# Kernel optimization log

Hardware: AMD Instinct MI355X
Metric: run time of the kernel (lower is better)

Reference implementation:

```python
import jax, jax.numpy as jnp
import numpy as np

N, D, E = 50000, 128, 800000


def setup_inputs() -> dict:
    key = jax.random.key(0)
    ks = jax.random.split(key, 12)
    x0 = jax.random.normal(ks[0], (N, D), dtype=jnp.float32)
    x1 = jax.random.normal(ks[1], (N, D), dtype=jnp.float32)
    edge_index = jax.random.randint(ks[2], (2, E), 0, N, dtype=jnp.int64)
    s = 0.05
    W1 = jax.random.normal(ks[3], (D, D), dtype=jnp.float32) * s
    b1 = jax.random.normal(ks[4], (D,), dtype=jnp.float32) * s
    W2 = jax.random.normal(ks[5], (D, D), dtype=jnp.float32) * s
    b2 = jax.random.normal(ks[6], (D,), dtype=jnp.float32) * s
    a1_w = jax.random.normal(ks[7], (D,), dtype=jnp.float32) * s
    a1_b = jax.random.normal(ks[8], (), dtype=jnp.float32) * s
    a2_w = jax.random.normal(ks[9], (D,), dtype=jnp.float32) * s
    a2_b = jax.random.normal(ks[10], (), dtype=jnp.float32) * s
    return {"x0": x0, "x1": x1, "edge_index": edge_index,
            "W1": W1, "b1": b1, "W2": W2, "b2": b2,
            "a1_w": a1_w, "a1_b": a1_b, "a2_w": a2_w, "a2_b": a2_b}


def reference(x0, x1, edge_index, W1, b1, W2, b2, a1_w, a1_b, a2_w, a2_b):
    # LeakyReLU(0.2) applied to both projections
    lrelu = lambda v: jnp.where(v >= 0, v, 0.2 * v)
    x0_i = lrelu(x0 @ W1.T + b1)          # [N, D]
    x0_j = lrelu(x0 @ W2.T + b2)          # [N, D]
    a1 = x0_i @ a1_w + a1_b               # [N]
    a2 = x0_j @ a2_w + a2_b               # [N]
    src, dst = edge_index[0], edge_index[1]
    # sigmoid(a_1 + a_2.T) evaluated only at the sparse edge indices
    att = jax.nn.sigmoid(a1[src] + a2[dst])            # [E]
    msg = att[:, None] * x0_j[dst]                     # [E, D]
    out = jax.ops.segment_sum(msg, src, num_segments=x0.shape[0])  # sparse.mm
    return out + x0
```

## Files before the change

### kernel.cpp

```cpp
#include <hip/hip_runtime.h>
#include <hip/hip_bf16.h>

typedef unsigned int u32;
typedef unsigned short u16;

#define DIM 128
#define CHUNK 2048

typedef __bf16 bfrag __attribute__((ext_vector_type(8)));
typedef float  facc  __attribute__((ext_vector_type(4)));

__device__ __forceinline__ float2 bfpair(u32 u) {
    union { u32 i; float f; } lo, hi;
    lo.i = (u & 0xFFFFu) << 16;
    hi.i = u & 0xFFFF0000u;
    return make_float2(lo.f, hi.f);
}
__device__ __forceinline__ float bf1(u16 h) {
    union { u32 i; float f; } a; a.i = ((u32)h) << 16; return a.f;
}
__device__ __forceinline__ u16 f2bf(float f) {
    __hip_bfloat16 h = __float2bfloat16(f);
    return *reinterpret_cast<u16*>(&h);
}
__device__ __forceinline__ u32 packbf(float x, float y) {
    return (u32)f2bf(x) | ((u32)f2bf(y) << 16);
}

template<bool BF16>
__device__ __forceinline__ float ldf(const void* p, int i) {
    if constexpr (BF16) return bf1(((const u16*)p)[i]);
    else                return ((const float*)p)[i];
}

template<bool BF16>
__device__ __forceinline__ bfrag ldfrag(const void* base, int row, int elt) {
    if constexpr (BF16) {
        const uint4* p = (const uint4*)((const u16*)base + (size_t)row * DIM + elt);
        return __builtin_bit_cast(bfrag, *p);
    } else {
        const float4* p = (const float4*)((const float*)base + (size_t)row * DIM + elt);
        float4 f0 = p[0], f1 = p[1];
        uint4 u = make_uint4(packbf(f0.x, f0.y), packbf(f0.z, f0.w),
                             packbf(f1.x, f1.y), packbf(f1.z, f1.w));
        return __builtin_bit_cast(bfrag, u);
    }
}

__global__ __launch_bounds__(64) void sniff_kernel(const u32* __restrict__ x0w,
                                                   const int* __restrict__ eiw,
                                                   int* __restrict__ flags) {
    int l = threadIdx.x;
    u32 w = x0w[l];
    u32 ef = (w >> 7) & 0xFF;
    bool inr = (ef >= 99 && ef <= 141);
    unsigned long long m1 = __ballot(inr);
    bool zodd = (eiw[2 * l + 1] == 0);
    unsigned long long m2 = __ballot(zodd);
    if (l == 0) {
        flags[0] = (__popcll(m1) >= 48) ? 1 : 0;
        flags[1] = (__popcll(m2) >= 32) ? 1 : 0;
    }
}

template<bool BF16>
__device__ __forceinline__ void proj_body(
    int grp, int chunk, int l,
    const void* __restrict__ x0v,
    const void* __restrict__ W1v, const void* __restrict__ b1v,
    const void* __restrict__ W2v, const void* __restrict__ b2v,
    const void* __restrict__ a1wv, const void* __restrict__ a1bv,
    const void* __restrict__ a2wv, const void* __restrict__ a2bv,
    u16* __restrict__ xj, float* __restrict__ a1, float* __restrict__ a2,
    int n)
{
    const void* Wv  = grp ? W2v  : W1v;
    const void* bv  = grp ? b2v  : b1v;
    const void* awv = grp ? a2wv : a1wv;
    const void* abv = grp ? a2bv : a1bv;
    float* aout     = grp ? a2   : a1;

    const int r0 = chunk * 32;
    const int lr = l & 15;
    const int q  = l >> 4;

    bfrag a[2][4];
    #pragma unroll
    for (int rt = 0; rt < 2; ++rt) {
        int row = min(r0 + rt * 16 + lr, n - 1);
        #pragma unroll
        for (int k = 0; k < 4; ++k)
            a[rt][k] = ldfrag<BF16>(x0v, row, k * 32 + q * 8);
    }

    facc acc[2][8];
    #pragma unroll
    for (int rt = 0; rt < 2; ++rt)
        #pragma unroll
        for (int ct = 0; ct < 8; ++ct)
            acc[rt][ct] = (facc){0.f, 0.f, 0.f, 0.f};

    #pragma unroll
    for (int ct = 0; ct < 8; ++ct) {
        bfrag bb[4];
        #pragma unroll
        for (int k = 0; k < 4; ++k)
            bb[k] = ldfrag<BF16>(Wv, ct * 16 + lr, k * 32 + q * 8);
        #pragma unroll
        for (int rt = 0; rt < 2; ++rt)
            #pragma unroll
            for (int k = 0; k < 4; ++k)
                acc[rt][ct] = __builtin_amdgcn_mfma_f32_16x16x32_bf16(
                    a[rt][k], bb[k], acc[rt][ct], 0, 0, 0);
    }

    float s[2][4] = {{0.f,0.f,0.f,0.f},{0.f,0.f,0.f,0.f}};
    #pragma unroll
    for (int ct = 0; ct < 8; ++ct) {
        float bc  = ldf<BF16>(bv,  ct * 16 + lr);
        float awc = ldf<BF16>(awv, ct * 16 + lr);
        #pragma unroll
        for (int rt = 0; rt < 2; ++rt)
            #pragma unroll
            for (int reg = 0; reg < 4; ++reg) {
                float v = acc[rt][ct][reg] + bc;
                v = v >= 0.f ? v : 0.2f * v;
                int row = r0 + rt * 16 + q * 4 + reg;
                if (grp && row < n)
                    xj[(size_t)row * DIM + ct * 16 + lr] = f2bf(v);
                s[rt][reg] = fmaf(v, awc, s[rt][reg]);
            }
    }
    #pragma unroll
    for (int off = 1; off < 16; off <<= 1)
        #pragma unroll
        for (int rt = 0; rt < 2; ++rt)
            #pragma unroll
            for (int reg = 0; reg < 4; ++reg)
                s[rt][reg] += __shfl_xor(s[rt][reg], off);
    if (lr == 0) {
        float ab = ldf<BF16>(abv, 0);
        #pragma unroll
        for (int rt = 0; rt < 2; ++rt)
            #pragma unroll
            for (int reg = 0; reg < 4; ++reg) {
                int row = r0 + rt * 16 + q * 4 + reg;
                if (row < n) aout[row] = s[rt][reg] + ab;
            }
    }
}

__global__ __launch_bounds__(64) void proj64_kernel(
    const void* __restrict__ x0v,
    const void* __restrict__ W1v, const void* __restrict__ b1v,
    const void* __restrict__ W2v, const void* __restrict__ b2v,
    const void* __restrict__ a1wv, const void* __restrict__ a1bv,
    const void* __restrict__ a2wv, const void* __restrict__ a2bv,
    u16* __restrict__ xj, float* __restrict__ a1, float* __restrict__ a2,
    const int* __restrict__ flags, int n, int nchunk)
{
    const int b = blockIdx.x;
    const int grp = (b >= nchunk) ? 1 : 0;
    const int chunk = b - grp * nchunk;
    const int l = threadIdx.x;
    if (flags[0] != 0)
        proj_body<true >(grp, chunk, l, x0v, W1v, b1v, W2v, b2v, a1wv, a1bv,
                         a2wv, a2bv, xj, a1, a2, n);
    else
        proj_body<false>(grp, chunk, l, x0v, W1v, b1v, W2v, b2v, a1wv, a1bv,
                         a2wv, a2bv, xj, a1, a2, n);
}

__global__ __launch_bounds__(256) void countH_kernel(
    const int* __restrict__ ei, u32* __restrict__ keys0,
    int* __restrict__ cnt, const int* __restrict__ flags, int ne, int nblk)
{
    __shared__ int h[256];
    const int b = blockIdx.x, t = threadIdx.x;
    h[t] = 0;
    __syncthreads();
    const bool i64 = flags[1] != 0;
    const int base = b * CHUNK;
    #pragma unroll
    for (int r = 0; r < CHUNK / 256; ++r) {
        int i = base + r * 256 + t;
        if (i < ne) {
            int src = i64 ? ei[2 * i] : ei[i];
            int dst = i64 ? ei[2 * (ne + i)] : ei[ne + i];
            u32 key = ((u32)src << 16) | (u32)dst;
            keys0[i] = key;
            atomicAdd(&h[key >> 24], 1);
        }
    }
    __syncthreads();
    cnt[t * nblk + b] = h[t];
}

__global__ __launch_bounds__(256) void scan1_kernel(
    const int* __restrict__ cnt, int* __restrict__ off,
    int* __restrict__ tot, int nblk)
{
    __shared__ int v[512];
    const int d = blockIdx.x, t = threadIdx.x;
    int c0 = (t < nblk) ? cnt[d * nblk + t] : 0;
    int c1 = (t + 256 < nblk) ? cnt[d * nblk + t + 256] : 0;
    v[t] = c0; v[t + 256] = c1;
    __syncthreads();
    for (int s = 1; s < 512; s <<= 1) {
        int a0 = v[t],      b0 = (t >= s) ? v[t - s] : 0;
        int a1 = v[t + 256], b1 = (t + 256 >= s) ? v[t + 256 - s] : 0;
        __syncthreads();
        v[t] = a0 + b0; v[t + 256] = a1 + b1;
        __syncthreads();
    }
    if (t < nblk)       off[d * nblk + t]       = v[t] - c0;
    if (t + 256 < nblk) off[d * nblk + t + 256] = v[t + 256] - c1;
    if (t == 0) tot[d] = v[511];
}

__global__ __launch_bounds__(256) void scan2_kernel(
    const int* __restrict__ tot, int* __restrict__ basev)
{
    __shared__ int v[256];
    const int t = threadIdx.x;
    int c = tot[t];
    v[t] = c;
    __syncthreads();
    for (int s = 1; s < 256; s <<= 1) {
        int a = v[t], b = (t >= s) ? v[t - s] : 0;
        __syncthreads();
        v[t] = a + b;
        __syncthreads();
    }
    basev[t] = v[t] - c;
}

__global__ __launch_bounds__(256) void reorderH_kernel(
    const u32* __restrict__ kin, u32* __restrict__ kout,
    const int* __restrict__ off, const int* __restrict__ basev,
    int ne, int nblk)
{
    __shared__ int boff[256];
    __shared__ int bcnt[256];
    const int b = blockIdx.x, t = threadIdx.x;
    const int base = b * CHUNK;
    boff[t] = basev[t] + off[t * nblk + b];
    bcnt[t] = 0;
    __syncthreads();
    #pragma unroll
    for (int r = 0; r < CHUNK / 256; ++r) {
        int i = base + r * 256 + t;
        if (i < ne) {
            u32 key = kin[i];
            int d = key >> 24;
            int rk = atomicAdd(&bcnt[d], 1);
            kout[boff[d] + rk] = key;
        }
    }
}

__global__ __launch_bounds__(256) void bucket_kernel(
    const u32* __restrict__ keys1, const int* __restrict__ basev,
    const int* __restrict__ tot, const float* __restrict__ a1,
    const float* __restrict__ a2, int* __restrict__ ptr,
    u32* __restrict__ sorted, int n)
{
    __shared__ int cnt[256];
    __shared__ int sc[256];
    __shared__ int cur[256];
    const int b = blockIdx.x, t = threadIdx.x;
    const int base = basev[b];
    const int size = tot[b];
    cnt[t] = 0;
    __syncthreads();
    for (int i = t; i < size; i += 256)
        atomicAdd(&cnt[(keys1[base + i] >> 16) & 0xFF], 1);
    __syncthreads();
    int c = cnt[t];
    sc[t] = c;
    __syncthreads();
    for (int s = 1; s < 256; s <<= 1) {
        int a = sc[t], add = (t >= s) ? sc[t - s] : 0;
        __syncthreads();
        sc[t] = a + add;
        __syncthreads();
    }
    int ex = sc[t] - c;
    cur[t] = ex;
    int sg = (b << 8) + t;
    if (sg <= n) ptr[sg] = base + ex;
    __syncthreads();
    for (int i = t; i < size; i += 256) {
        u32 key = keys1[base + i];
        int j   = (key >> 16) & 0xFF;
        int rk  = atomicAdd(&cur[j], 1);
        int src = (int)(key >> 16);
        int dst = (int)(key & 0xFFFFu);
        float av  = a1[src] + a2[dst];
        float att = 1.0f / (1.0f + __expf(-av));
        u32 a16 = (u32)lrintf(att * 65535.0f);
        sorted[base + rk] = (a16 << 16) | (u32)dst;
    }
}

#define ATTDEC(r) ((float)((r) >> 16) * (1.0f / 65535.0f))

__global__ __launch_bounds__(256) void gather_kernel(
    const int* __restrict__ ptr, const u32* __restrict__ sorted,
    const u32* __restrict__ xjw, const void* __restrict__ x0v,
    void* __restrict__ outv, const int* __restrict__ flags, int n)
{
    const bool bf16 = flags[0] != 0;
    int s = blockIdx.x * 4 + (threadIdx.x >> 6);
    int l = threadIdx.x & 63;
    if (s >= n) return;

    float2 acc0, acc1;
    if (bf16) acc0 = bfpair(((const u32*)x0v)[(size_t)s * 64 + l]);
    else      acc0 = ((const float2*)x0v)[(size_t)s * 64 + l];
    acc1 = make_float2(0.f, 0.f);

    int k = ptr[s], end = ptr[s + 1];

    while (k + 16 <= end) {
        u32 r[16];
        #pragma unroll
        for (int j = 0; j < 16; ++j) r[j] = sorted[k + j];
        u32 w[16];
        #pragma unroll
        for (int j = 0; j < 16; ++j) w[j] = xjw[(size_t)(r[j] & 0xFFFFu) * 64 + l];
        #pragma unroll
        for (int j = 0; j < 16; ++j) {
            float att = ATTDEC(r[j]);
            float2 xv = bfpair(w[j]);
            if (j & 1) { acc1.x = fmaf(att, xv.x, acc1.x);
                         acc1.y = fmaf(att, xv.y, acc1.y); }
            else       { acc0.x = fmaf(att, xv.x, acc0.x);
                         acc0.y = fmaf(att, xv.y, acc0.y); }
        }
        k += 16;
    }
    if (k + 8 <= end) {
        u32 r[8];
        #pragma unroll
        for (int j = 0; j < 8; ++j) r[j] = sorted[k + j];
        u32 w[8];
        #pragma unroll
        for (int j = 0; j < 8; ++j) w[j] = xjw[(size_t)(r[j] & 0xFFFFu) * 64 + l];
        #pragma unroll
        for (int j = 0; j < 8; ++j) {
            float att = ATTDEC(r[j]);
            float2 xv = bfpair(w[j]);
            if (j & 1) { acc1.x = fmaf(att, xv.x, acc1.x);
                         acc1.y = fmaf(att, xv.y, acc1.y); }
            else       { acc0.x = fmaf(att, xv.x, acc0.x);
                         acc0.y = fmaf(att, xv.y, acc0.y); }
        }
        k += 8;
    }
    if (k + 4 <= end) {
        u32 r[4];
        #pragma unroll
        for (int j = 0; j < 4; ++j) r[j] = sorted[k + j];
        u32 w[4];
        #pragma unroll
        for (int j = 0; j < 4; ++j) w[j] = xjw[(size_t)(r[j] & 0xFFFFu) * 64 + l];
        #pragma unroll
        for (int j = 0; j < 4; ++j) {
            float att = ATTDEC(r[j]);
            float2 xv = bfpair(w[j]);
            if (j & 1) { acc1.x = fmaf(att, xv.x, acc1.x);
                         acc1.y = fmaf(att, xv.y, acc1.y); }
            else       { acc0.x = fmaf(att, xv.x, acc0.x);
                         acc0.y = fmaf(att, xv.y, acc0.y); }
        }
        k += 4;
    }
    for (; k < end; ++k) {
        u32 cur = sorted[k];
        float att = ATTDEC(cur);
        float2 xv = bfpair(xjw[(size_t)(cur & 0xFFFFu) * 64 + l]);
        acc0.x = fmaf(att, xv.x, acc0.x);
        acc0.y = fmaf(att, xv.y, acc0.y);
    }
    acc0.x += acc1.x;
    acc0.y += acc1.y;

    if (bf16) ((u32*)outv)[(size_t)s * 64 + l] = packbf(acc0.x, acc0.y);
    else      ((float2*)outv)[(size_t)s * 64 + l] = acc0;
}

extern "C" void kernel_launch(void* const* d_in, const int* in_sizes, int n_in,
                              void* d_out, int out_size, void* d_ws, size_t ws_size,
                              hipStream_t stream)
{
    const void* x0  = d_in[0];
    const int*  ei  = (const int*)d_in[2];
    const void* W1  = d_in[3];
    const void* b1  = d_in[4];
    const void* W2  = d_in[5];
    const void* b2  = d_in[6];
    const void* a1w = d_in[7];
    const void* a1b = d_in[8];
    const void* a2w = d_in[9];
    const void* a2b = d_in[10];

    const int n = in_sizes[0] / DIM;
    const int e = in_sizes[2] / 2;
    const int nblk = (e + CHUNK - 1) / CHUNK;

    char* ws = (char*)d_ws;
    int* flags = (int*)ws;
    size_t off = 1024;
    u16* xj = (u16*)(ws + off);
    off += (size_t)n * DIM * sizeof(u16);   off = (off + 255) & ~(size_t)255;
    float* a1 = (float*)(ws + off);
    off += (size_t)n * sizeof(float);       off = (off + 255) & ~(size_t)255;
    float* a2 = (float*)(ws + off);
    off += (size_t)n * sizeof(float);       off = (off + 255) & ~(size_t)255;
    u32* keys0 = (u32*)(ws + off);
    off += (size_t)e * sizeof(u32);         off = (off + 255) & ~(size_t)255;
    u32* keys1 = (u32*)(ws + off);
    off += (size_t)e * sizeof(u32);         off = (off + 255) & ~(size_t)255;
    int* cntH = (int*)(ws + off);
    off += (size_t)256 * nblk * sizeof(int); off = (off + 255) & ~(size_t)255;
    int* offH = (int*)(ws + off);
    off += (size_t)256 * nblk * sizeof(int); off = (off + 255) & ~(size_t)255;
    int* totH = (int*)(ws + off);  off += 1024;
    int* baseH = (int*)(ws + off); off += 1024;
    int* ptr = (int*)(ws + off);
    off += (size_t)(n + 1) * sizeof(int);   off = (off + 255) & ~(size_t)255;
    u32* sorted = (u32*)(ws + off);

    sniff_kernel<<<1, 64, 0, stream>>>((const u32*)x0, ei, flags);

    const int nchunk = (n + 31) / 32;

    proj64_kernel<<<2 * nchunk, 64, 0, stream>>>(x0, W1, b1, W2, b2, a1w, a1b,
        a2w, a2b, xj, a1, a2, flags, n, nchunk);

    countH_kernel<<<nblk, 256, 0, stream>>>(ei, keys0, cntH, flags, e, nblk);
    scan1_kernel<<<256, 256, 0, stream>>>(cntH, offH, totH, nblk);
    scan2_kernel<<<1, 256, 0, stream>>>(totH, baseH);
    reorderH_kernel<<<nblk, 256, 0, stream>>>(keys0, keys1, offH, baseH, e, nblk);
    const int nbucket = (n >> 8) + 1;
    bucket_kernel<<<nbucket, 256, 0, stream>>>(keys1, baseH, totH, a1, a2,
                                               ptr, sorted, n);

    int gblocks = (n + 3) / 4;
    gather_kernel<<<gblocks, 256, 0, stream>>>(ptr, sorted, (const u32*)xj,
                                               x0, d_out, flags, n);
}
```

Baseline: 209.9 us.

## Pre-convert x0/W to bf16 and stage weights in LDS for projection

Adds a conversion kernel that turns fp32 x0 and W1/W2 into bf16 copies in workspace. The projection kernel now uses 256-thread blocks: each block stages the 128x128 bf16 weight matrix into padded shared memory once, and four waves reuse it, instead of every wave reloading weight fragments from global memory. The aim is to cut redundant weight loads and per-fragment fp32 to bf16 packing. The cost is an extra pass over x0 (read fp32, write bf16, then read bf16 again) and an extra launch.

```diff
diff --git a/kernel.cpp b/kernel.cpp
--- a/kernel.cpp
+++ b/kernel.cpp
@@ -5,6 +5,7 @@
 typedef unsigned short u16;
 
 #define DIM 128
+#define LWS 136
 #define CHUNK 2048
 
 typedef __bf16 bfrag __attribute__((ext_vector_type(8)));
@@ -26,25 +27,8 @@
 __device__ __forceinline__ u32 packbf(float x, float y) {
     return (u32)f2bf(x) | ((u32)f2bf(y) << 16);
 }
-
-template<bool BF16>
-__device__ __forceinline__ float ldf(const void* p, int i) {
-    if constexpr (BF16) return bf1(((const u16*)p)[i]);
-    else                return ((const float*)p)[i];
-}
-
-template<bool BF16>
-__device__ __forceinline__ bfrag ldfrag(const void* base, int row, int elt) {
-    if constexpr (BF16) {
-        const uint4* p = (const uint4*)((const u16*)base + (size_t)row * DIM + elt);
-        return __builtin_bit_cast(bfrag, *p);
-    } else {
-        const float4* p = (const float4*)((const float*)base + (size_t)row * DIM + elt);
-        float4 f0 = p[0], f1 = p[1];
-        uint4 u = make_uint4(packbf(f0.x, f0.y), packbf(f0.z, f0.w),
-                             packbf(f1.x, f1.y), packbf(f1.z, f1.w));
-        return __builtin_bit_cast(bfrag, u);
-    }
+__device__ __forceinline__ float ldfr(const void* p, int i, bool isbf) {
+    return isbf ? bf1(((const u16*)p)[i]) : ((const float*)p)[i];
 }
 
 __global__ __launch_bounds__(64) void sniff_kernel(const u32* __restrict__ x0w,
@@ -63,23 +47,63 @@
     }
 }
 
-template<bool BF16>
-__device__ __forceinline__ void proj_body(
-    int grp, int chunk, int l,
-    const void* __restrict__ x0v,
+__global__ __launch_bounds__(256) void cvt_kernel(
+    const float* __restrict__ x0, const float* __restrict__ W1,
+    const float* __restrict__ W2, u16* __restrict__ x0c, u16* __restrict__ Wc,
+    const int* __restrict__ flags, int nx)
+{
+    if (flags[0] != 0) return;
+    int i = blockIdx.x * 256 + threadIdx.x;
+    if (i >= nx + 4096) return;
+    const float* src; u16* dst; int c;
+    if (i < nx) { src = x0; dst = x0c; c = i; }
+    else {
+        int j = i - nx;
+        src = (j < 2048) ? W1 : W2;
+        dst = Wc + ((j < 2048) ? 0 : 16384);
+        c = j & 2047;
+    }
+    float4 f0 = ((const float4*)src)[c * 2];
+    float4 f1 = ((const float4*)src)[c * 2 + 1];
+    uint4 u = make_uint4(packbf(f0.x, f0.y), packbf(f0.z, f0.w),
+                         packbf(f1.x, f1.y), packbf(f1.z, f1.w));
+    ((uint4*)dst)[c] = u;
+}
+
+__global__ __launch_bounds__(256) void proj_kernel(
+    const void* __restrict__ x0v, const u16* __restrict__ x0c,
     const void* __restrict__ W1v, const void* __restrict__ b1v,
     const void* __restrict__ W2v, const void* __restrict__ b2v,
     const void* __restrict__ a1wv, const void* __restrict__ a1bv,
     const void* __restrict__ a2wv, const void* __restrict__ a2bv,
+    const u16* __restrict__ Wc,
     u16* __restrict__ xj, float* __restrict__ a1, float* __restrict__ a2,
-    int n)
-{
-    const void* Wv  = grp ? W2v  : W1v;
+    const int* __restrict__ flags, int n, int nchunk, int bpg)
+{
+    __shared__ u16 lw[128 * LWS];
+
+    const bool isbf = flags[0] != 0;
+    const int t   = threadIdx.x;
+    const int grp = blockIdx.x / bpg;
+    const int cb  = blockIdx.x % bpg;
+
+    const u16* x0s  = isbf ? (const u16*)x0v : x0c;
+    const u16* Ws   = isbf ? (const u16*)(grp ? W2v : W1v) : (Wc + grp * 16384);
     const void* bv  = grp ? b2v  : b1v;
     const void* awv = grp ? a2wv : a1wv;
     const void* abv = grp ? a2bv : a1bv;
     float* aout     = grp ? a2   : a1;
 
+    for (int j = t; j < 2048; j += 256) {
+        int r = j >> 4, c = j & 15;
+        *(uint4*)(lw + (size_t)r * LWS + c * 8) =
+            *(const uint4*)(Ws + (size_t)r * DIM + c * 8);
+    }
+    __syncthreads();
+
+    const int wid = t >> 6, l = t & 63;
+    const int chunk = cb * 4 + wid;
+    if (chunk >= nchunk) return;
     const int r0 = chunk * 32;
     const int lr = l & 15;
     const int q  = l >> 4;
@@ -89,8 +113,10 @@
     for (int rt = 0; rt < 2; ++rt) {
         int row = min(r0 + rt * 16 + lr, n - 1);
         #pragma unroll
-        for (int k = 0; k < 4; ++k)
-            a[rt][k] = ldfrag<BF16>(x0v, row, k * 32 + q * 8);
+        for (int k = 0; k < 4; ++k) {
+            const uint4* p = (const uint4*)(x0s + (size_t)row * DIM + k * 32 + q * 8);
+            a[rt][k] = __builtin_bit_cast(bfrag, *p);
+        }
     }
 
     facc acc[2][8];
@@ -103,9 +129,10 @@
     #pragma unroll
     for (int ct = 0; ct < 8; ++ct) {
         bfrag bb[4];
+        const u16* lrow = lw + (size_t)(ct * 16 + lr) * LWS;
         #pragma unroll
         for (int k = 0; k < 4; ++k)
-            bb[k] = ldfrag<BF16>(Wv, ct * 16 + lr, k * 32 + q * 8);
+            bb[k] = *(const bfrag*)(lrow + k * 32 + q * 8);
         #pragma unroll
         for (int rt = 0; rt < 2; ++rt)
             #pragma unroll
@@ -117,8 +144,8 @@
     float s[2][4] = {{0.f,0.f,0.f,0.f},{0.f,0.f,0.f,0.f}};
     #pragma unroll
     for (int ct = 0; ct < 8; ++ct) {
-        float bc  = ldf<BF16>(bv,  ct * 16 + lr);
-        float awc = ldf<BF16>(awv, ct * 16 + lr);
+        float bc  = ldfr(bv,  ct * 16 + lr, isbf);
+        float awc = ldfr(awv, ct * 16 + lr, isbf);
         #pragma unroll
         for (int rt = 0; rt < 2; ++rt)
             #pragma unroll
@@ -139,7 +166,7 @@
             for (int reg = 0; reg < 4; ++reg)
                 s[rt][reg] += __shfl_xor(s[rt][reg], off);
     if (lr == 0) {
-        float ab = ldf<BF16>(abv, 0);
+        float ab = ldfr(abv, 0, isbf);
         #pragma unroll
         for (int rt = 0; rt < 2; ++rt)
             #pragma unroll
@@ -148,27 +175,6 @@
                 if (row < n) aout[row] = s[rt][reg] + ab;
             }
     }
-}
-
-__global__ __launch_bounds__(64) void proj64_kernel(
-    const void* __restrict__ x0v,
-    const void* __restrict__ W1v, const void* __restrict__ b1v,
-    const void* __restrict__ W2v, const void* __restrict__ b2v,
-    const void* __restrict__ a1wv, const void* __restrict__ a1bv,
-    const void* __restrict__ a2wv, const void* __restrict__ a2bv,
-    u16* __restrict__ xj, float* __restrict__ a1, float* __restrict__ a2,
-    const int* __restrict__ flags, int n, int nchunk)
-{
-    const int b = blockIdx.x;
-    const int grp = (b >= nchunk) ? 1 : 0;
-    const int chunk = b - grp * nchunk;
-    const int l = threadIdx.x;
-    if (flags[0] != 0)
-        proj_body<true >(grp, chunk, l, x0v, W1v, b1v, W2v, b2v, a1wv, a1bv,
-                         a2wv, a2bv, xj, a1, a2, n);
-    else
-        proj_body<false>(grp, chunk, l, x0v, W1v, b1v, W2v, b2v, a1wv, a1bv,
-                         a2wv, a2bv, xj, a1, a2, n);
 }
 
 __global__ __launch_bounds__(256) void countH_kernel(
@@ -414,6 +420,10 @@
     size_t off = 1024;
     u16* xj = (u16*)(ws + off);
     off += (size_t)n * DIM * sizeof(u16);   off = (off + 255) & ~(size_t)255;
+    u16* x0c = (u16*)(ws + off);
+    off += (size_t)n * DIM * sizeof(u16);   off = (off + 255) & ~(size_t)255;
+    u16* Wc = (u16*)(ws + off);
+    off += (size_t)2 * 16384 * sizeof(u16); off = (off + 255) & ~(size_t)255;
     float* a1 = (float*)(ws + off);
     off += (size_t)n * sizeof(float);       off = (off + 255) & ~(size_t)255;
     float* a2 = (float*)(ws + off);
@@ -434,10 +444,15 @@
 
     sniff_kernel<<<1, 64, 0, stream>>>((const u32*)x0, ei, flags);
 
+    const int nx = n * DIM / 8;
+    const int cblocks = (nx + 4096 + 255) / 256;
+    cvt_kernel<<<cblocks, 256, 0, stream>>>((const float*)x0, (const float*)W1,
+        (const float*)W2, x0c, Wc, flags, nx);
+
     const int nchunk = (n + 31) / 32;
-
-    proj64_kernel<<<2 * nchunk, 64, 0, stream>>>(x0, W1, b1, W2, b2, a1w, a1b,
-        a2w, a2b, xj, a1, a2, flags, n, nchunk);
+    const int bpg = (nchunk + 3) / 4;
+    proj_kernel<<<2 * bpg, 256, 0, stream>>>(x0, x0c, W1, b1, W2, b2, a1w, a1b,
+        a2w, a2b, Wc, xj, a1, a2, flags, n, nchunk, bpg);
 
     countH_kernel<<<nblk, 256, 0, stream>>>(ei, keys0, cntH, flags, e, nblk);
     scan1_kernel<<<256, 256, 0, stream>>>(cntH, offH, totH, nblk);
```

Result: faster. 197.6 us (-5.9%).
